# Kernel tuning notes

Hardware: AMD Instinct MI355X
Metric: run time of the kernel (lower is better)

## Reference

```python
import jax, jax.numpy as jnp
import numpy as np

K = 3
PAD = 1


def _deform_conv(x, offset, weight, bias):
    """torchvision-style deform_conv2d (v1, no mask), stride=1, pad=1, dil=1.
    x: [B,C,H,W], offset: [B,2*K*K,H,W] ordered (dy,dx) per kernel pos (row-major).
    """
    B, C, H, W = x.shape
    K2 = K * K
    off = offset.reshape(B, K2, 2, H, W)
    dy, dx = off[:, :, 0], off[:, :, 1]
    ky = jnp.repeat(jnp.arange(K), K).astype(x.dtype)  # [K2] kernel row offsets
    kx = jnp.tile(jnp.arange(K), K).astype(x.dtype)    # [K2] kernel col offsets
    hh = jnp.arange(H, dtype=x.dtype)
    ww = jnp.arange(W, dtype=x.dtype)
    # sampling positions: [B,K2,H,W]
    py = hh[None, None, :, None] + ky[None, :, None, None] - PAD + dy
    px = ww[None, None, None, :] + kx[None, :, None, None] - PAD + dx
    y0f = jnp.floor(py)
    x0f = jnp.floor(px)
    wy = py - y0f
    wx = px - x0f
    y0 = y0f.astype(jnp.int32)
    x0 = x0f.astype(jnp.int32)
    xf = x.reshape(B, C, H * W)

    def corner(iy, ix, w):
        # zero padding outside the image: contribution masked to 0
        valid = (iy >= 0) & (iy < H) & (ix >= 0) & (ix < W)
        iyc = jnp.clip(iy, 0, H - 1)
        ixc = jnp.clip(ix, 0, W - 1)
        lin = (iyc * W + ixc).reshape(B, -1)                      # [B,K2*H*W]
        g = jnp.take_along_axis(xf, lin[:, None, :], axis=2)     # [B,C,K2*H*W]
        g = g.reshape(B, C, K2, H, W)
        wv = (w * valid.astype(x.dtype))[:, None]                # [B,1,K2,H,W]
        return g * wv

    val = (corner(y0, x0, (1 - wy) * (1 - wx))
           + corner(y0, x0 + 1, (1 - wy) * wx)
           + corner(y0 + 1, x0, wy * (1 - wx))
           + corner(y0 + 1, x0 + 1, wy * wx))                    # [B,C,K2,H,W]
    O = weight.shape[0]
    out = jnp.einsum('ock,bckhw->bohw', weight.reshape(O, C, K2), val)
    return out + bias[None, :, None, None]


def setup_inputs() -> dict:
    key = jax.random.key(0)
    k1, k2, k3, k4, k5 = jax.random.split(key, 5)
    B, C, O, H, W = 4, 64, 64, 128, 128
    fan = C * K * K
    x = jax.random.normal(k1, (B, C, H, W), dtype=jnp.float32)
    w_off = jax.random.normal(k2, (2 * K * K, C, K, K), dtype=jnp.float32) / np.sqrt(fan)
    b_off = jax.random.normal(k3, (2 * K * K,), dtype=jnp.float32) * 0.01
    w_dcn = jax.random.normal(k4, (O, C, K, K), dtype=jnp.float32) / np.sqrt(fan)
    b_dcn = jax.random.normal(k5, (O,), dtype=jnp.float32) * 0.01
    return {"x": x, "w_off": w_off, "b_off": b_off, "w_dcn": w_dcn, "b_dcn": b_dcn}


def reference(x, w_off, b_off, w_dcn, b_dcn):
    offset = jax.lax.conv_general_dilated(
        x, w_off, window_strides=(1, 1), padding=((PAD, PAD), (PAD, PAD)),
        dimension_numbers=('NCHW', 'OIHW', 'NCHW')) + b_off[None, :, None, None]
    return _deform_conv(x, offset, w_dcn, b_dcn)
```

## Files before the change

### kernel.cpp

```cpp
#include <hip/hip_runtime.h>

#define HH 128
#define WW 128
#define CC 64
#define OO 64
#define HWSZ (HH*WW)

typedef short bf16x8 __attribute__((ext_vector_type(8)));
typedef float f32x4  __attribute__((ext_vector_type(4)));

__device__ __forceinline__ unsigned short f2bf(float f) {
    unsigned u = __float_as_uint(f);
    u = (u + 0x7FFFu + ((u >> 16) & 1u)) >> 16;
    return (unsigned short)u;
}
__device__ __forceinline__ float bf2f(unsigned short s) {
    return __uint_as_float(((unsigned)s) << 16);
}

__global__ __launch_bounds__(256) void transpose_x(const float* __restrict__ x,
                                                   unsigned short* __restrict__ xhb) {
    __shared__ float tile[64 * 65];
    int w0 = blockIdx.x * 64, h = blockIdx.y, b = blockIdx.z;
    int t = threadIdx.x;
    const float* xb = x + ((long)b * CC * HWSZ) + h * WW + w0;
#pragma unroll
    for (int i = 0; i < 16; ++i) {
        int idx = i * 256 + t; int c = idx >> 6, w = idx & 63;
        tile[c * 65 + w] = xb[c * HWSZ + w];
    }
    __syncthreads();
    unsigned short* xo = xhb + ((long)((b * HH + h) * WW + w0)) * CC;
#pragma unroll
    for (int i = 0; i < 8; ++i) {
        int idx = i * 256 + t; int w = idx >> 5, c = (idx & 31) * 2;
        ushort2 u;
        u.x = f2bf(tile[c * 65 + w]);
        u.y = f2bf(tile[(c + 1) * 65 + w]);
        *(ushort2*)(xo + w * CC + c) = u;
    }
}

__global__ __launch_bounds__(256) void prep_w(const float* __restrict__ wd,
                                              const float* __restrict__ wo,
                                              unsigned short* __restrict__ wdt,
                                              unsigned short* __restrict__ wot) {
    int i = blockIdx.x * 256 + threadIdx.x;
    if (i < 9 * 64 * 64) {
        int k = i >> 12, r = i & 4095, o = r >> 6, c = r & 63;
        wdt[i] = f2bf(wd[(o * 64 + c) * 9 + k]);
    }
    int j = i - 9 * 64 * 64;
    if (j >= 0 && j < 9 * 32 * 64) {
        int k = j >> 11, r = j & 2047, oc = r >> 6, c = r & 63;
        wot[j] = f2bf(oc < 18 ? wo[(oc * 64 + c) * 9 + k] : 0.0f);
    }
}

__global__ __launch_bounds__(256) void offset_tile(const unsigned short* __restrict__ xhb,
                                                   const unsigned short* __restrict__ wot,
                                                   const float* __restrict__ b_off,
                                                   float* __restrict__ ofb) {
    __shared__ unsigned short xr[3 * 68 * 72];
    int w0 = blockIdx.x * 64, h = blockIdx.y, b = blockIdx.z;
    int t = threadIdx.x;

#pragma unroll
    for (int i = 0; i < 7; ++i) {
        int idx = i * 256 + t;
        if (idx < 1584) {
            int r = idx / 528;
            int rem = idx - r * 528;
            int p = rem >> 3, cc = rem & 7;
            int y = h + r - 1, wx = w0 - 1 + p;
            uint4 v = make_uint4(0u, 0u, 0u, 0u);
            if (((unsigned)y < HH) && ((unsigned)wx < WW))
                v = *(const uint4*)(xhb + ((long)((b * HH + y) * WW + wx)) * CC + cc * 8);
            *(uint4*)&xr[(r * 68 + p) * 72 + cc * 8] = v;
        }
    }
    __syncthreads();

    int l = t & 63, wv = t >> 6;
    int m = l & 15, q = l >> 4;
    int px0 = wv * 16;
    f32x4 acc0 = {0.f, 0.f, 0.f, 0.f}, acc1 = {0.f, 0.f, 0.f, 0.f};

#pragma unroll
    for (int k = 0; k < 9; ++k) {
        int ky = k / 3, kx = k - ky * 3;
        const unsigned short* ar = &xr[(ky * 68 + px0 + m + kx) * 72 + q * 8];
        bf16x8 a0 = *(const bf16x8*)(ar);
        bf16x8 a1 = *(const bf16x8*)(ar + 32);
        const unsigned short* bp = wot + k * 2048 + q * 8;
        bf16x8 b00 = *(const bf16x8*)(bp + m * 64);
        bf16x8 b01 = *(const bf16x8*)(bp + m * 64 + 32);
        bf16x8 b10 = *(const bf16x8*)(bp + (16 + m) * 64);
        bf16x8 b11 = *(const bf16x8*)(bp + (16 + m) * 64 + 32);
        acc0 = __builtin_amdgcn_mfma_f32_16x16x32_bf16(a0, b00, acc0, 0, 0, 0);
        acc0 = __builtin_amdgcn_mfma_f32_16x16x32_bf16(a1, b01, acc0, 0, 0, 0);
        acc1 = __builtin_amdgcn_mfma_f32_16x16x32_bf16(a0, b10, acc1, 0, 0, 0);
        acc1 = __builtin_amdgcn_mfma_f32_16x16x32_bf16(a1, b11, acc1, 0, 0, 0);
    }
    float* dst = ofb + ((long)((b * HH + h) * WW + w0 + px0)) * 18;
    float bo0 = b_off[m];
#pragma unroll
    for (int r = 0; r < 4; ++r)
        dst[(q * 4 + r) * 18 + m] = acc0[r] + bo0;
    if (m < 2) {
        float bo1 = b_off[16 + m];
#pragma unroll
        for (int r = 0; r < 4; ++r)
            dst[(q * 4 + r) * 18 + 16 + m] = acc1[r] + bo1;
    }
}

__global__ __launch_bounds__(256) void deform_tile(const unsigned short* __restrict__ xhb,
                                                   const float* __restrict__ ofb,
                                                   const unsigned short* __restrict__ wdt,
                                                   const float* __restrict__ b_dcn,
                                                   float* __restrict__ out) {
    __shared__ unsigned short lds[4 * 64 * 72];
    unsigned short* vbuf[2] = { lds,             lds + 2 * 64 * 72 };
    unsigned short* wbuf[2] = { lds + 64 * 72,   lds + 3 * 64 * 72 };

    int w0 = blockIdx.x * 64, h = blockIdx.y, b = blockIdx.z;
    int t = threadIdx.x;
    int l = t & 63, wv = t >> 6;
    int m = l & 15, q = l >> 4;
    int spx = t >> 2, q4 = t & 3;

    const unsigned short* xb = xhb + (long)b * HWSZ * CC;

    float2 o9[9];
    {
        const float* op = ofb + ((long)((b * HH + h) * WW + w0 + spx)) * 18;
#pragma unroll
        for (int k = 0; k < 9; ++k) o9[k] = *(const float2*)(op + 2 * k);
    }

    f32x4 acc[4];
#pragma unroll
    for (int i = 0; i < 4; ++i) acc[i] = f32x4{0.f, 0.f, 0.f, 0.f};

    auto stage = [&](int k, unsigned short* vb, unsigned short* wb) {
        {
            const unsigned short* wsrc = wdt + k * 4096;
            int o = t >> 2, cc = (t & 3) * 2;
            uint4 wv0 = *(const uint4*)(wsrc + o * 64 + cc * 8);
            uint4 wv1 = *(const uint4*)(wsrc + o * 64 + cc * 8 + 8);
            *(uint4*)&wb[o * 72 + cc * 8] = wv0;
            *(uint4*)&wb[o * 72 + cc * 8 + 8] = wv1;
        }
        int ky = k / 3, kx = k - ky * 3;
        float py  = (float)(h + ky - 1) + o9[k].x;
        float pxf = (float)(w0 + spx + kx - 1) + o9[k].y;
        float y0f = floorf(py), x0f = floorf(pxf);
        float wy = py - y0f, wx = pxf - x0f;
        int y0 = (int)y0f, x0 = (int)x0f, y1 = y0 + 1, x1 = x0 + 1;
        bool vy0 = (unsigned)y0 < HH, vy1 = (unsigned)y1 < HH;
        bool vx0 = (unsigned)x0 < WW, vx1 = (unsigned)x1 < WW;
        int y0c = min(max(y0, 0), HH - 1), y1c = min(max(y1, 0), HH - 1);
        int x0c = min(max(x0, 0), WW - 1), x1c = min(max(x1, 0), WW - 1);
        float cw0 = (vy0 && vx0) ? (1.f - wy) * (1.f - wx) : 0.f;
        float cw1 = (vy0 && vx1) ? (1.f - wy) * wx : 0.f;
        float cw2 = (vy1 && vx0) ? wy * (1.f - wx) : 0.f;
        float cw3 = (vy1 && vx1) ? wy * wx : 0.f;
        const unsigned short* p00 = xb + (y0c * WW + x0c) * CC + q4 * 16;
        const unsigned short* p01 = xb + (y0c * WW + x1c) * CC + q4 * 16;
        const unsigned short* p10 = xb + (y1c * WW + x0c) * CC + q4 * 16;
        const unsigned short* p11 = xb + (y1c * WW + x1c) * CC + q4 * 16;
        bf16x8 s00a = *(const bf16x8*)p00,      s00b = *(const bf16x8*)(p00 + 8);
        bf16x8 s01a = *(const bf16x8*)p01,      s01b = *(const bf16x8*)(p01 + 8);
        bf16x8 s10a = *(const bf16x8*)p10,      s10b = *(const bf16x8*)(p10 + 8);
        bf16x8 s11a = *(const bf16x8*)p11,      s11b = *(const bf16x8*)(p11 + 8);
        bf16x8 a0, a1;
#pragma unroll
        for (int e = 0; e < 8; ++e) {
            float v = cw0 * bf2f((unsigned short)s00a[e])
                    + cw1 * bf2f((unsigned short)s01a[e])
                    + cw2 * bf2f((unsigned short)s10a[e])
                    + cw3 * bf2f((unsigned short)s11a[e]);
            a0[e] = (short)f2bf(v);
            float u = cw0 * bf2f((unsigned short)s00b[e])
                    + cw1 * bf2f((unsigned short)s01b[e])
                    + cw2 * bf2f((unsigned short)s10b[e])
                    + cw3 * bf2f((unsigned short)s11b[e]);
            a1[e] = (short)f2bf(u);
        }
        *(bf16x8*)&vb[spx * 72 + q4 * 16] = a0;
        *(bf16x8*)&vb[spx * 72 + q4 * 16 + 8] = a1;
    };

    stage(0, vbuf[0], wbuf[0]);
    __syncthreads();

#pragma unroll
    for (int k = 0; k < 9; ++k) {
        if (k < 8) stage(k + 1, vbuf[(k + 1) & 1], wbuf[(k + 1) & 1]);

        const unsigned short* vb = vbuf[k & 1];
        const unsigned short* wb = wbuf[k & 1];
        const unsigned short* ap = &vb[(wv * 16 + m) * 72 + q * 8];
        bf16x8 a0 = *(const bf16x8*)(ap);
        bf16x8 a1 = *(const bf16x8*)(ap + 32);
#pragma unroll
        for (int ot = 0; ot < 4; ++ot) {
            const unsigned short* bp = &wb[(ot * 16 + m) * 72 + q * 8];
            bf16x8 b0 = *(const bf16x8*)(bp);
            bf16x8 b1 = *(const bf16x8*)(bp + 32);
            acc[ot] = __builtin_amdgcn_mfma_f32_16x16x32_bf16(a0, b0, acc[ot], 0, 0, 0);
            acc[ot] = __builtin_amdgcn_mfma_f32_16x16x32_bf16(a1, b1, acc[ot], 0, 0, 0);
        }
        __syncthreads();
    }

#pragma unroll
    for (int ot = 0; ot < 4; ++ot) {
        int o = ot * 16 + m;
        float bo = b_dcn[o];
        f32x4 r = acc[ot];
        r[0] += bo; r[1] += bo; r[2] += bo; r[3] += bo;
        float* dst = out + ((long)(b * OO + o)) * HWSZ + h * WW + w0 + wv * 16 + q * 4;
        *(f32x4*)dst = r;
    }
}

extern "C" void kernel_launch(void* const* d_in, const int* in_sizes, int n_in,
                              void* d_out, int out_size, void* d_ws, size_t ws_size,
                              hipStream_t stream) {
    const float* x     = (const float*)d_in[0];
    const float* w_off = (const float*)d_in[1];
    const float* b_off = (const float*)d_in[2];
    const float* w_dcn = (const float*)d_in[3];
    const float* b_dcn = (const float*)d_in[4];
    float* out = (float*)d_out;

    char* ws = (char*)d_ws;
    unsigned short* xhb = (unsigned short*)ws;
    float*          ofb = (float*)(ws + 8388608);
    unsigned short* wdt = (unsigned short*)(ws + 13107200);
    unsigned short* wot = (unsigned short*)(ws + 13180928);

    hipLaunchKernelGGL(transpose_x, dim3(2, 128, 4), dim3(256), 0, stream, x, xhb);
    hipLaunchKernelGGL(prep_w, dim3(216), dim3(256), 0, stream, w_dcn, w_off, wdt, wot);
    hipLaunchKernelGGL(offset_tile, dim3(2, 128, 4), dim3(256), 0, stream,
                       xhb, wot, b_off, ofb);
    hipLaunchKernelGGL(deform_tile, dim3(2, 128, 4), dim3(256), 0, stream,
                       xhb, ofb, wdt, b_dcn, out);
}
```

Before: 126.2 us.

## Switch to fp16, load weights from global, split gather into issue/commit

The intermediate activations and weights move from bf16 to fp16, and the MFMA instructions change to their f16 variants. In deform_tile the weights are no longer staged through LDS each tap; each lane reads its B fragments straight from global/L2. The bilinear gather is split into an issue phase, which starts the global loads before the MFMAs, and a commit phase after the MFMAs that blends and writes to LDS, so gather latency overlaps compute. This halves LDS use and adds a launch-bounds occupancy hint, at the cost of more registers held live across the MFMAs and redundant global weight reads.

```diff
diff --git a/kernel.cpp b/kernel.cpp
--- a/kernel.cpp
+++ b/kernel.cpp
@@ -1,4 +1,5 @@
 #include <hip/hip_runtime.h>
+#include <hip/hip_fp16.h>
 
 #define HH 128
 #define WW 128
@@ -6,20 +7,15 @@
 #define OO 64
 #define HWSZ (HH*WW)
 
-typedef short bf16x8 __attribute__((ext_vector_type(8)));
-typedef float f32x4  __attribute__((ext_vector_type(4)));
-
-__device__ __forceinline__ unsigned short f2bf(float f) {
-    unsigned u = __float_as_uint(f);
-    u = (u + 0x7FFFu + ((u >> 16) & 1u)) >> 16;
-    return (unsigned short)u;
-}
-__device__ __forceinline__ float bf2f(unsigned short s) {
-    return __uint_as_float(((unsigned)s) << 16);
+typedef _Float16 f16x8 __attribute__((ext_vector_type(8)));
+typedef float    f32x4 __attribute__((ext_vector_type(4)));
+
+__device__ __forceinline__ unsigned short f2h(float f) {
+    return __half_as_ushort(__float2half_rn(f));
 }
 
 __global__ __launch_bounds__(256) void transpose_x(const float* __restrict__ x,
-                                                   unsigned short* __restrict__ xhb) {
+                                                   unsigned short* __restrict__ xh) {
     __shared__ float tile[64 * 65];
     int w0 = blockIdx.x * 64, h = blockIdx.y, b = blockIdx.z;
     int t = threadIdx.x;
@@ -30,13 +26,13 @@
         tile[c * 65 + w] = xb[c * HWSZ + w];
     }
     __syncthreads();
-    unsigned short* xo = xhb + ((long)((b * HH + h) * WW + w0)) * CC;
+    unsigned short* xo = xh + ((long)((b * HH + h) * WW + w0)) * CC;
 #pragma unroll
     for (int i = 0; i < 8; ++i) {
         int idx = i * 256 + t; int w = idx >> 5, c = (idx & 31) * 2;
         ushort2 u;
-        u.x = f2bf(tile[c * 65 + w]);
-        u.y = f2bf(tile[(c + 1) * 65 + w]);
+        u.x = f2h(tile[c * 65 + w]);
+        u.y = f2h(tile[(c + 1) * 65 + w]);
         *(ushort2*)(xo + w * CC + c) = u;
     }
 }
@@ -48,16 +44,16 @@
     int i = blockIdx.x * 256 + threadIdx.x;
     if (i < 9 * 64 * 64) {
         int k = i >> 12, r = i & 4095, o = r >> 6, c = r & 63;
-        wdt[i] = f2bf(wd[(o * 64 + c) * 9 + k]);
+        wdt[i] = f2h(wd[(o * 64 + c) * 9 + k]);
     }
     int j = i - 9 * 64 * 64;
     if (j >= 0 && j < 9 * 32 * 64) {
         int k = j >> 11, r = j & 2047, oc = r >> 6, c = r & 63;
-        wot[j] = f2bf(oc < 18 ? wo[(oc * 64 + c) * 9 + k] : 0.0f);
-    }
-}
-
-__global__ __launch_bounds__(256) void offset_tile(const unsigned short* __restrict__ xhb,
+        wot[j] = f2h(oc < 18 ? wo[(oc * 64 + c) * 9 + k] : 0.0f);
+    }
+}
+
+__global__ __launch_bounds__(256) void offset_tile(const unsigned short* __restrict__ xh,
                                                    const unsigned short* __restrict__ wot,
                                                    const float* __restrict__ b_off,
                                                    float* __restrict__ ofb) {
@@ -75,7 +71,7 @@
             int y = h + r - 1, wx = w0 - 1 + p;
             uint4 v = make_uint4(0u, 0u, 0u, 0u);
             if (((unsigned)y < HH) && ((unsigned)wx < WW))
-                v = *(const uint4*)(xhb + ((long)((b * HH + y) * WW + wx)) * CC + cc * 8);
+                v = *(const uint4*)(xh + ((long)((b * HH + y) * WW + wx)) * CC + cc * 8);
             *(uint4*)&xr[(r * 68 + p) * 72 + cc * 8] = v;
         }
     }
@@ -90,17 +86,17 @@
     for (int k = 0; k < 9; ++k) {
         int ky = k / 3, kx = k - ky * 3;
         const unsigned short* ar = &xr[(ky * 68 + px0 + m + kx) * 72 + q * 8];
-        bf16x8 a0 = *(const bf16x8*)(ar);
-        bf16x8 a1 = *(const bf16x8*)(ar + 32);
+        f16x8 a0 = *(const f16x8*)(ar);
+        f16x8 a1 = *(const f16x8*)(ar + 32);
         const unsigned short* bp = wot + k * 2048 + q * 8;
-        bf16x8 b00 = *(const bf16x8*)(bp + m * 64);
-        bf16x8 b01 = *(const bf16x8*)(bp + m * 64 + 32);
-        bf16x8 b10 = *(const bf16x8*)(bp + (16 + m) * 64);
-        bf16x8 b11 = *(const bf16x8*)(bp + (16 + m) * 64 + 32);
-        acc0 = __builtin_amdgcn_mfma_f32_16x16x32_bf16(a0, b00, acc0, 0, 0, 0);
-        acc0 = __builtin_amdgcn_mfma_f32_16x16x32_bf16(a1, b01, acc0, 0, 0, 0);
-        acc1 = __builtin_amdgcn_mfma_f32_16x16x32_bf16(a0, b10, acc1, 0, 0, 0);
-        acc1 = __builtin_amdgcn_mfma_f32_16x16x32_bf16(a1, b11, acc1, 0, 0, 0);
+        f16x8 b00 = *(const f16x8*)(bp + m * 64);
+        f16x8 b01 = *(const f16x8*)(bp + m * 64 + 32);
+        f16x8 b10 = *(const f16x8*)(bp + (16 + m) * 64);
+        f16x8 b11 = *(const f16x8*)(bp + (16 + m) * 64 + 32);
+        acc0 = __builtin_amdgcn_mfma_f32_16x16x32_f16(a0, b00, acc0, 0, 0, 0);
+        acc0 = __builtin_amdgcn_mfma_f32_16x16x32_f16(a1, b01, acc0, 0, 0, 0);
+        acc1 = __builtin_amdgcn_mfma_f32_16x16x32_f16(a0, b10, acc1, 0, 0, 0);
+        acc1 = __builtin_amdgcn_mfma_f32_16x16x32_f16(a1, b11, acc1, 0, 0, 0);
     }
     float* dst = ofb + ((long)((b * HH + h) * WW + w0 + px0)) * 18;
     float bo0 = b_off[m];
@@ -115,14 +111,12 @@
     }
 }
 
-__global__ __launch_bounds__(256) void deform_tile(const unsigned short* __restrict__ xhb,
-                                                   const float* __restrict__ ofb,
-                                                   const unsigned short* __restrict__ wdt,
-                                                   const float* __restrict__ b_dcn,
-                                                   float* __restrict__ out) {
-    __shared__ unsigned short lds[4 * 64 * 72];
-    unsigned short* vbuf[2] = { lds,             lds + 2 * 64 * 72 };
-    unsigned short* wbuf[2] = { lds + 64 * 72,   lds + 3 * 64 * 72 };
+__global__ __launch_bounds__(256, 4) void deform_tile(const unsigned short* __restrict__ xh,
+                                                      const float* __restrict__ ofb,
+                                                      const unsigned short* __restrict__ wdt,
+                                                      const float* __restrict__ b_dcn,
+                                                      float* __restrict__ out) {
+    __shared__ unsigned short vs[2][64 * 72];
 
     int w0 = blockIdx.x * 64, h = blockIdx.y, b = blockIdx.z;
     int t = threadIdx.x;
@@ -130,7 +124,7 @@
     int m = l & 15, q = l >> 4;
     int spx = t >> 2, q4 = t & 3;
 
-    const unsigned short* xb = xhb + (long)b * HWSZ * CC;
+    const unsigned short* xb = xh + (long)b * HWSZ * CC;
 
     float2 o9[9];
     {
@@ -143,15 +137,10 @@
 #pragma unroll
     for (int i = 0; i < 4; ++i) acc[i] = f32x4{0.f, 0.f, 0.f, 0.f};
 
-    auto stage = [&](int k, unsigned short* vb, unsigned short* wb) {
-        {
-            const unsigned short* wsrc = wdt + k * 4096;
-            int o = t >> 2, cc = (t & 3) * 2;
-            uint4 wv0 = *(const uint4*)(wsrc + o * 64 + cc * 8);
-            uint4 wv1 = *(const uint4*)(wsrc + o * 64 + cc * 8 + 8);
-            *(uint4*)&wb[o * 72 + cc * 8] = wv0;
-            *(uint4*)&wb[o * 72 + cc * 8 + 8] = wv1;
-        }
+    f16x8 c00a, c00b, c01a, c01b, c10a, c10b, c11a, c11b;
+    float cw0, cw1, cw2, cw3;
+
+    auto issue = [&](int k) {
         int ky = k / 3, kx = k - ky * 3;
         float py  = (float)(h + ky - 1) + o9[k].x;
         float pxf = (float)(w0 + spx + kx - 1) + o9[k].y;
@@ -162,56 +151,66 @@
         bool vx0 = (unsigned)x0 < WW, vx1 = (unsigned)x1 < WW;
         int y0c = min(max(y0, 0), HH - 1), y1c = min(max(y1, 0), HH - 1);
         int x0c = min(max(x0, 0), WW - 1), x1c = min(max(x1, 0), WW - 1);
-        float cw0 = (vy0 && vx0) ? (1.f - wy) * (1.f - wx) : 0.f;
-        float cw1 = (vy0 && vx1) ? (1.f - wy) * wx : 0.f;
-        float cw2 = (vy1 && vx0) ? wy * (1.f - wx) : 0.f;
-        float cw3 = (vy1 && vx1) ? wy * wx : 0.f;
+        cw0 = (vy0 && vx0) ? (1.f - wy) * (1.f - wx) : 0.f;
+        cw1 = (vy0 && vx1) ? (1.f - wy) * wx : 0.f;
+        cw2 = (vy1 && vx0) ? wy * (1.f - wx) : 0.f;
+        cw3 = (vy1 && vx1) ? wy * wx : 0.f;
         const unsigned short* p00 = xb + (y0c * WW + x0c) * CC + q4 * 16;
         const unsigned short* p01 = xb + (y0c * WW + x1c) * CC + q4 * 16;
         const unsigned short* p10 = xb + (y1c * WW + x0c) * CC + q4 * 16;
         const unsigned short* p11 = xb + (y1c * WW + x1c) * CC + q4 * 16;
-        bf16x8 s00a = *(const bf16x8*)p00,      s00b = *(const bf16x8*)(p00 + 8);
-        bf16x8 s01a = *(const bf16x8*)p01,      s01b = *(const bf16x8*)(p01 + 8);
-        bf16x8 s10a = *(const bf16x8*)p10,      s10b = *(const bf16x8*)(p10 + 8);
-        bf16x8 s11a = *(const bf16x8*)p11,      s11b = *(const bf16x8*)(p11 + 8);
-        bf16x8 a0, a1;
+        c00a = *(const f16x8*)p00;  c00b = *(const f16x8*)(p00 + 8);
+        c01a = *(const f16x8*)p01;  c01b = *(const f16x8*)(p01 + 8);
+        c10a = *(const f16x8*)p10;  c10b = *(const f16x8*)(p10 + 8);
+        c11a = *(const f16x8*)p11;  c11b = *(const f16x8*)(p11 + 8);
+    };
+    auto commit = [&](unsigned short* vb) {
+        f16x8 a0, a1;
 #pragma unroll
         for (int e = 0; e < 8; ++e) {
-            float v = cw0 * bf2f((unsigned short)s00a[e])
-                    + cw1 * bf2f((unsigned short)s01a[e])
-                    + cw2 * bf2f((unsigned short)s10a[e])
-                    + cw3 * bf2f((unsigned short)s11a[e]);
-            a0[e] = (short)f2bf(v);
-            float u = cw0 * bf2f((unsigned short)s00b[e])
-                    + cw1 * bf2f((unsigned short)s01b[e])
-                    + cw2 * bf2f((unsigned short)s10b[e])
-                    + cw3 * bf2f((unsigned short)s11b[e]);
-            a1[e] = (short)f2bf(u);
+            float v = cw0 * (float)c00a[e] + cw1 * (float)c01a[e]
+                    + cw2 * (float)c10a[e] + cw3 * (float)c11a[e];
+            a0[e] = (_Float16)v;
+            float u = cw0 * (float)c00b[e] + cw1 * (float)c01b[e]
+                    + cw2 * (float)c10b[e] + cw3 * (float)c11b[e];
+            a1[e] = (_Float16)u;
         }
-        *(bf16x8*)&vb[spx * 72 + q4 * 16] = a0;
-        *(bf16x8*)&vb[spx * 72 + q4 * 16 + 8] = a1;
+        *(f16x8*)&vb[spx * 72 + q4 * 16] = a0;
+        *(f16x8*)&vb[spx * 72 + q4 * 16 + 8] = a1;
     };
 
-    stage(0, vbuf[0], wbuf[0]);
+    issue(0);
+    commit(&vs[0][0]);
     __syncthreads();
 
 #pragma unroll
     for (int k = 0; k < 9; ++k) {
-        if (k < 8) stage(k + 1, vbuf[(k + 1) & 1], wbuf[(k + 1) & 1]);
-
-        const unsigned short* vb = vbuf[k & 1];
-        const unsigned short* wb = wbuf[k & 1];
-        const unsigned short* ap = &vb[(wv * 16 + m) * 72 + q * 8];
-        bf16x8 a0 = *(const bf16x8*)(ap);
-        bf16x8 a1 = *(const bf16x8*)(ap + 32);
-#pragma unroll
-        for (int ot = 0; ot < 4; ++ot) {
-            const unsigned short* bp = &wb[(ot * 16 + m) * 72 + q * 8];
-            bf16x8 b0 = *(const bf16x8*)(bp);
-            bf16x8 b1 = *(const bf16x8*)(bp + 32);
-            acc[ot] = __builtin_amdgcn_mfma_f32_16x16x32_bf16(a0, b0, acc[ot], 0, 0, 0);
-            acc[ot] = __builtin_amdgcn_mfma_f32_16x16x32_bf16(a1, b1, acc[ot], 0, 0, 0);
-        }
+        if (k < 8) issue(k + 1);
+
+        const unsigned short* bp = wdt + k * 4096 + q * 8;
+        f16x8 bf0 = *(const f16x8*)(bp + (0 * 16 + m) * 64);
+        f16x8 bf1 = *(const f16x8*)(bp + (0 * 16 + m) * 64 + 32);
+        f16x8 bf2 = *(const f16x8*)(bp + (1 * 16 + m) * 64);
+        f16x8 bf3 = *(const f16x8*)(bp + (1 * 16 + m) * 64 + 32);
+        f16x8 bf4 = *(const f16x8*)(bp + (2 * 16 + m) * 64);
+        f16x8 bf5 = *(const f16x8*)(bp + (2 * 16 + m) * 64 + 32);
+        f16x8 bf6 = *(const f16x8*)(bp + (3 * 16 + m) * 64);
+        f16x8 bf7 = *(const f16x8*)(bp + (3 * 16 + m) * 64 + 32);
+
+        const unsigned short* ap = &vs[k & 1][(wv * 16 + m) * 72 + q * 8];
+        f16x8 a0 = *(const f16x8*)(ap);
+        f16x8 a1 = *(const f16x8*)(ap + 32);
+
+        acc[0] = __builtin_amdgcn_mfma_f32_16x16x32_f16(a0, bf0, acc[0], 0, 0, 0);
+        acc[0] = __builtin_amdgcn_mfma_f32_16x16x32_f16(a1, bf1, acc[0], 0, 0, 0);
+        acc[1] = __builtin_amdgcn_mfma_f32_16x16x32_f16(a0, bf2, acc[1], 0, 0, 0);
+        acc[1] = __builtin_amdgcn_mfma_f32_16x16x32_f16(a1, bf3, acc[1], 0, 0, 0);
+        acc[2] = __builtin_amdgcn_mfma_f32_16x16x32_f16(a0, bf4, acc[2], 0, 0, 0);
+        acc[2] = __builtin_amdgcn_mfma_f32_16x16x32_f16(a1, bf5, acc[2], 0, 0, 0);
+        acc[3] = __builtin_amdgcn_mfma_f32_16x16x32_f16(a0, bf6, acc[3], 0, 0, 0);
+        acc[3] = __builtin_amdgcn_mfma_f32_16x16x32_f16(a1, bf7, acc[3], 0, 0, 0);
+
+        if (k < 8) commit(&vs[(k + 1) & 1][0]);
         __syncthreads();
     }
 
@@ -237,15 +236,15 @@
     float* out = (float*)d_out;
 
     char* ws = (char*)d_ws;
-    unsigned short* xhb = (unsigned short*)ws;
+    unsigned short* xh  = (unsigned short*)ws;
     float*          ofb = (float*)(ws + 8388608);
     unsigned short* wdt = (unsigned short*)(ws + 13107200);
     unsigned short* wot = (unsigned short*)(ws + 13180928);
 
-    hipLaunchKernelGGL(transpose_x, dim3(2, 128, 4), dim3(256), 0, stream, x, xhb);
+    hipLaunchKernelGGL(transpose_x, dim3(2, 128, 4), dim3(256), 0, stream, x, xh);
     hipLaunchKernelGGL(prep_w, dim3(216), dim3(256), 0, stream, w_dcn, w_off, wdt, wot);
     hipLaunchKernelGGL(offset_tile, dim3(2, 128, 4), dim3(256), 0, stream,
-                       xhb, wot, b_off, ofb);
+                       xh, wot, b_off, ofb);
     hipLaunchKernelGGL(deform_tile, dim3(2, 128, 4), dim3(256), 0, stream,
-                       xhb, ofb, wdt, b_dcn, out);
-}
+                       xh, ofb, wdt, b_dcn, out);
+}
```

Measured after the change: 150.1 us. 18.9% more time.
